# Kernel tuning notes

Hardware: AMD Instinct MI355X
Metric: run time of the kernel (lower is better)

Reference implementation:

```python
import jax, jax.numpy as jnp
import numpy as np

EPS = 1e-5
BLOCKS = 8

def _bn(x, g, b, m, v):
    # eval-mode BatchNorm1d over channel dim of [B, C, T]
    return g[:, None] * (x - m[:, None]) * jax.lax.rsqrt(v[:, None] + EPS) + b[:, None]

def _conv1x1(x, w):
    # x: [B, Cin, T], w: [Cout, Cin] -> [B, Cout, T]
    return jnp.einsum('bct,oc->bot', x, w)

def _dwconv(x, w, dil):
    # x: [B, C, T], w: [C, K] depthwise dilated conv, 'same' padding
    C, K = w.shape
    pad = dil * (K - 1) // 2
    return jax.lax.conv_general_dilated(
        x, w[:, None, :], window_strides=(1,), padding=[(pad, pad)],
        rhs_dilation=(dil,), dimension_numbers=('NCH', 'OIH', 'NCH'),
        feature_group_count=C)

def setup_inputs() -> dict:
    key = jax.random.key(0)
    ks = jax.random.split(key, 16)
    B, Cb, H, T, K = 16, 256, 512, 4096, 3
    d = {}
    d['x'] = jax.random.normal(ks[0], (B, Cb, T), jnp.float32)
    d['bn1_gamma'] = jax.random.uniform(ks[1], (BLOCKS, Cb), jnp.float32)
    d['bn1_beta'] = jax.random.normal(ks[2], (BLOCKS, Cb), jnp.float32)
    d['bn1_mean'] = jax.random.normal(ks[3], (BLOCKS, Cb), jnp.float32)
    d['bn1_var'] = jax.random.uniform(ks[4], (BLOCKS, Cb), jnp.float32)
    d['w1'] = jax.random.normal(ks[5], (BLOCKS, H, Cb), jnp.float32)
    d['bn2_gamma'] = jax.random.uniform(ks[6], (BLOCKS, H), jnp.float32)
    d['bn2_beta'] = jax.random.normal(ks[7], (BLOCKS, H), jnp.float32)
    d['bn2_mean'] = jax.random.normal(ks[8], (BLOCKS, H), jnp.float32)
    d['bn2_var'] = jax.random.uniform(ks[9], (BLOCKS, H), jnp.float32)
    d['dw_w'] = jax.random.normal(ks[10], (BLOCKS, H, K), jnp.float32)
    d['bn3_gamma'] = jax.random.uniform(ks[11], (BLOCKS, H), jnp.float32)
    d['bn3_beta'] = jax.random.normal(ks[12], (BLOCKS, H), jnp.float32)
    d['bn3_mean'] = jax.random.normal(ks[13], (BLOCKS, H), jnp.float32)
    d['bn3_var'] = jax.random.uniform(ks[14], (BLOCKS, H), jnp.float32)
    d['w2'] = jax.random.normal(ks[15], (BLOCKS, Cb, H), jnp.float32)
    return d

def reference(x, bn1_gamma, bn1_beta, bn1_mean, bn1_var, w1,
              bn2_gamma, bn2_beta, bn2_mean, bn2_var, dw_w,
              bn3_gamma, bn3_beta, bn3_mean, bn3_var, w2):
    sign = jnp.sign  # binary activation on inputs and weights
    resid = x
    for i in range(BLOCKS):
        dil = 2 ** i
        h = _bn(resid, bn1_gamma[i], bn1_beta[i], bn1_mean[i], bn1_var[i])
        h = _conv1x1(sign(h), sign(w1[i]))                 # 1x1, Cb -> H
        h = _bn(h, bn2_gamma[i], bn2_beta[i], bn2_mean[i], bn2_var[i])
        h = _dwconv(sign(h), sign(dw_w[i]), dil)           # depthwise dilated
        h = _bn(h, bn3_gamma[i], bn3_beta[i], bn3_mean[i], bn3_var[i])
        h = _conv1x1(sign(h), sign(w2[i]))                 # 1x1, H -> Cb
        resid = resid + h
    return resid
```

## Files before the change

### kernel.cpp

```cpp
#include <hip/hip_runtime.h>
#include <stdint.h>

namespace {
constexpr int Bn  = 16;
constexpr int Cc  = 256;
constexpr int Hn  = 512;
constexpr int Tn  = 4096;
constexpr int CWn = Cc / 32;
constexpr int HWn = Hn / 32;
constexpr int TWn = Tn / 32;
constexpr int TC  = 64;
constexpr float EPSf = 1e-5f;
}

typedef __attribute__((ext_vector_type(4)))  int i32x4;
typedef __attribute__((ext_vector_type(16))) int i32x16;

__global__ __launch_bounds__(256) void setup_kernel(
    const float* __restrict__ bn1g, const float* __restrict__ bn1b,
    const float* __restrict__ bn1m, const float* __restrict__ bn1v,
    const float* __restrict__ w1,
    const float* __restrict__ bn2g, const float* __restrict__ bn2b,
    const float* __restrict__ bn2m, const float* __restrict__ bn2v,
    const float* __restrict__ dww,
    const float* __restrict__ bn3g, const float* __restrict__ bn3b,
    const float* __restrict__ bn3m, const float* __restrict__ bn3v,
    const float* __restrict__ w2,
    float* __restrict__ thr1, float* __restrict__ thr2, float* __restrict__ thr3,
    uint32_t* __restrict__ dws, uint32_t* __restrict__ W1p,
    uint8_t* __restrict__ W1f, int* __restrict__ Sw1, int* __restrict__ T2i,
    uint8_t* __restrict__ W2uf, int* __restrict__ Sw2)
{
  const int idx = blockIdx.x * 256 + threadIdx.x;
  if (idx < 8 * Hn * CWn) {
    const int w = idx & (CWn - 1);
    const int h = idx >> 3;
    const float* src = w1 + (size_t)h * Cc + w * 32;
    uint32_t word = 0;
#pragma unroll
    for (int j = 0; j < 32; ++j) word |= (uint32_t)(src[j] > 0.f) << j;
    W1p[h * CWn + w] = word;
    atomicAdd(&Sw1[h], (int)__popc(word));
    const int blk = h >> 9, hl = h & 511;
    uint32_t* dst = (uint32_t*)(W1f + (size_t)blk * 131072);
#pragma unroll
    for (int q = 0; q < 8; ++q) {
      const uint32_t dw = (((word >> (4 * q)) & 0xFu) * 0x00204081u) & 0x01010101u;
      dst[((w * 2 + (q >> 2)) * 512 + hl) * 4 + (q & 3)] = dw;
    }
  } else {
    const int k = idx - 8 * Hn * CWn;
    const int w = k & (HWn - 1);
    const int c = k >> 4;
    const float* src = w2 + (size_t)c * Hn + w * 32;
    uint32_t word = 0;
#pragma unroll
    for (int j = 0; j < 32; ++j) word |= (uint32_t)(src[j] > 0.f) << j;
    atomicAdd(&Sw2[c], (int)__popc(word));
    const int blk = c >> 8, cl = c & 255;
    uint32_t* dst = (uint32_t*)(W2uf + (size_t)blk * 131072);
#pragma unroll
    for (int q = 0; q < 8; ++q) {
      const uint32_t dw = (((word >> (4 * q)) & 0xFu) * 0x00204081u) & 0x01010101u;
      dst[((w * 2 + (q >> 2)) * 256 + cl) * 4 + (q & 3)] = dw;
    }
  }
  if (idx < 8 * Cc)
    thr1[idx] = bn1m[idx] - bn1b[idx] * sqrtf(bn1v[idx] + EPSf) / bn1g[idx];
  if (idx < 8 * Hn) {
    const float th2 = bn2m[idx] - bn2b[idx] * sqrtf(bn2v[idx] + EPSf) / bn2g[idx];
    thr2[idx] = th2;
    int T;
    if (th2 >= 8.0e6f)       T =  (1 << 24);
    else if (th2 <= -8.0e6f) T = -(1 << 24);
    else if (th2 == th2)     T = (int)floorf(th2) + 1;
    else                     T =  (1 << 24);
    T2i[idx] = T;
    thr3[idx] = bn3m[idx] - bn3b[idx] * sqrtf(bn3v[idx] + EPSf) / bn3g[idx];
    uint32_t dw = 0;
    for (int k2 = 0; k2 < 3; ++k2) dw |= (uint32_t)(dww[(size_t)idx * 3 + k2] > 0.f) << k2;
    dws[idx] = dw;
  }
}

__global__ __launch_bounds__(256) void k1_pack(
    const float* __restrict__ resid, const float* __restrict__ thr1,
    uint32_t* __restrict__ Xp)
{
  const int idx = blockIdx.x * 256 + threadIdx.x;
  const int t  = idx & (Tn - 1);
  const int cw = (idx >> 12) & (CWn - 1);
  const int b  = idx >> 15;
  const float* r = resid + ((size_t)(b * Cc + cw * 32)) * Tn + t;
  uint32_t word = 0;
#pragma unroll
  for (int j = 0; j < 32; ++j)
    word |= (uint32_t)(r[(size_t)j * Tn] > thr1[cw * 32 + j]) << j;
  Xp[((size_t)b * CWn + cw) * Tn + t] = word;
}

__global__ __launch_bounds__(256) void k2_gemm1(
    const uint32_t* __restrict__ Xp, const uint32_t* __restrict__ W1p,
    const float* __restrict__ thr2, uint32_t* __restrict__ Y)
{
  const int bid  = blockIdx.x;
  const int tblk = bid & 15;
  const int og   = (bid >> 4) & 63;
  const int b    = bid >> 10;
  const int t    = tblk * 256 + threadIdx.x;
  const int o    = og * 8;

  const uint32_t* xrow = Xp + (size_t)b * CWn * Tn + t;
  const uint32_t* wrow = W1p + o * CWn;
  int acc[8] = {0, 0, 0, 0, 0, 0, 0, 0};
#pragma unroll
  for (int w = 0; w < CWn; ++w) {
    const uint32_t xw = xrow[(size_t)w * Tn];
#pragma unroll
    for (int r = 0; r < 8; ++r)
      acc[r] += __popc(xw ^ wrow[r * CWn + w]);
  }
  const int lane = threadIdx.x & 63;
#pragma unroll
  for (int r = 0; r < 8; ++r) {
    const float v = (float)(Cc - 2 * acc[r]);
    const uint64_t m = __ballot(v > thr2[o + r]);
    if ((lane & 31) == 0)
      Y[((size_t)b * TWn + (t >> 5)) * Hn + o + r] = (uint32_t)(m >> lane);
  }
}

__global__ __launch_bounds__(512) void k_iter(
    const uint32_t* __restrict__ Yin, const uint32_t* __restrict__ dws,
    const float* __restrict__ thr3,
    const uint8_t* __restrict__ W2uf, const int* __restrict__ Sw2_i,
    const float* __restrict__ rin, float* __restrict__ rout,
    const float* __restrict__ thr1n,
    const uint8_t* __restrict__ W1f_n, const int* __restrict__ Sw1_n,
    const int* __restrict__ T2i_n, uint32_t* __restrict__ Yout,
    int dil, int do_next)
{
  __shared__ __align__(16) uint8_t Zi8[TC * 512];
  __shared__ __align__(16) uint8_t Xi8[TC * 256];
  __shared__ int   Tc[Hn];
  __shared__ float thr1L[Cc];
  __shared__ int   Sw2x2L[Cc];
  __shared__ int   Sx[TC], Sz[TC];

  const int chunk = blockIdx.x & (Tn / TC - 1);
  const int b     = blockIdx.x >> 6;
  const int tid   = threadIdx.x;
  const int lane  = tid & 63;
  const int wid   = __builtin_amdgcn_readfirstlane(tid >> 6);
  const int lh    = lane & 31;
  const int twL   = lane >> 5;
  const int tw0   = chunk * 2;
  const int half  = lane >> 5;

  float rv0[16], rv1[16];
  {
    const int t0 = chunk * TC;
#pragma unroll
    for (int r = 0; r < 16; ++r) {
      const int cr = wid * 32 + (r & 3) + 8 * (r >> 2) + 4 * half;
      const float* rowp = rin + ((size_t)(b * Cc + cr)) * Tn + t0;
      rv0[r] = rowp[lh];
      rv1[r] = rowp[32 + lh];
    }
  }

  if (tid < TC) { Sx[tid] = 0; Sz[tid] = 0; }
  if (tid < Cc) { thr1L[tid] = thr1n[tid]; Sw2x2L[tid] = 2 * Sw2_i[tid]; }
  Tc[tid] = T2i_n[tid] + 2 * Sw1_n[tid] - 256;
  __syncthreads();

  int zcnt = 0;
#pragma unroll
  for (int task = 0; task < 2; ++task) {
    const int hw = wid * 2 + task;
    const int tw = tw0 + twL;
    const int ch = hw * 32 + lh;

    const uint32_t* yb = Yin + (size_t)b * TWn * Hn + ch;
    const uint32_t ycur = yb[(size_t)tw * Hn];
    uint32_t yl, yr, Vl, Vr;
    if (dil >= 32) {
      const int dw = dil >> 5;
      const bool lok = tw >= dw, rok = tw + dw < TWn;
      yl = lok ? yb[(size_t)(tw - dw) * Hn] : 0u;
      yr = rok ? yb[(size_t)(tw + dw) * Hn] : 0u;
      Vl = lok ? ~0u : 0u;
      Vr = rok ? ~0u : 0u;
    } else {
      const uint32_t yp = (tw > 0) ? yb[(size_t)(tw - 1) * Hn] : 0u;
      const uint32_t yn = (tw < TWn - 1) ? yb[(size_t)(tw + 1) * Hn] : 0u;
      yl = (ycur << dil) | ((tw > 0) ? (yp >> (32 - dil)) : 0u);
      yr = (ycur >> dil) | ((tw < TWn - 1) ? (yn << (32 - dil)) : 0u);
      Vl = (tw == 0) ? (~0u << dil) : ~0u;
      Vr = (tw == TWn - 1) ? (~0u >> dil) : ~0u;
    }
    const uint32_t d = dws[ch];
    const uint32_t a  = ((d & 1u) ? yl : ~yl) & Vl;
    const uint32_t bb = (d & 2u) ? ycur : ~ycur;
    const uint32_t c  = ((d & 4u) ? yr : ~yr) & Vr;

    const float thr = thr3[ch];
    const float v3 = (thr + 3.f) * 0.5f;
    const float v2 = (thr + 2.f) * 0.5f;
    const int K3 = (int)(v3 >= 0.f) + (int)(v3 >= 1.f) + (int)(v3 >= 2.f) + (int)(v3 >= 3.f);
    const int K2 = (int)(v2 >= 0.f) + (int)(v2 >= 1.f) + (int)(v2 >= 2.f);

    const uint32_t g1 = a | bb | c;
    const uint32_t g2 = (a & bb) | (c & (a | bb));
    const uint32_t g3 = a & bb & c;
    const uint32_t full = (K3 == 0) ? ~0u : (K3 == 1) ? g1 : (K3 == 2) ? g2
                        : (K3 == 3) ? g3 : 0u;
    const uint32_t lm = (K2 == 0) ? ~0u : (K2 == 1) ? (bb | c) : (K2 == 2) ? (bb & c) : 0u;
    const uint32_t rm = (K2 == 0) ? ~0u : (K2 == 1) ? (a | bb) : (K2 == 2) ? (a & bb) : 0u;

    uint32_t w = (Vl & Vr & full) | (~Vl & lm) | (~Vr & rm);

#pragma unroll
    for (int s = 16; s; s >>= 1) {
      const uint32_t m = 0xFFFFFFFFu / ((1u << s) + 1u);
      const uint32_t o = __shfl_xor(w, s, 64);
      w = ((lane & s) == 0) ? ((w & m) | ((o & m) << s))
                            : ((w & ~m) | ((o & ~m) >> s));
    }
    const int swzA = (lane & 15) << 4;
    uint32_t e[8];
#pragma unroll
    for (int q = 0; q < 8; ++q)
      e[q] = (((w >> (4 * q)) & 0xFu) * 0x00204081u) & 0x01010101u;
    i32x4 v0; v0[0] = e[0]; v0[1] = e[1]; v0[2] = e[2]; v0[3] = e[3];
    i32x4 v1; v1[0] = e[4]; v1[1] = e[5]; v1[2] = e[6]; v1[3] = e[7];
    *(i32x4*)&Zi8[lane * 512 + ((hw * 32)      ^ swzA)] = v0;
    *(i32x4*)&Zi8[lane * 512 + ((hw * 32 + 16) ^ swzA)] = v1;
    zcnt += (int)__popc(w);
  }
  atomicAdd(&Sz[lane], zcnt);
  __syncthreads();

  {
    const int mc   = wid;
    const int lrow = mc * 32 + lh;
    const int t0   = chunk * TC;

    const int swz0 = (lh & 15) << 4;
    i32x16 acc0 = {0,0,0,0, 0,0,0,0, 0,0,0,0, 0,0,0,0};
    i32x16 acc1 = {0,0,0,0, 0,0,0,0, 0,0,0,0, 0,0,0,0};
#pragma unroll
    for (int kg = 0; kg < 2; ++kg) {
      i32x4 afv[8];
#pragma unroll
      for (int kk = 0; kk < 8; ++kk) {
        const int ks = kg * 8 + kk;
        afv[kk] = *(const i32x4*)(W2uf + (((size_t)(ks * 2 + half) * 256 + lrow) * 16));
      }
#pragma unroll
      for (int kk = 0; kk < 8; ++kk) {
        const int ks = kg * 8 + kk;
        const int k0 = ks * 32 + half * 16;
        const i32x4 bf0 = *(const i32x4*)&Zi8[lh * 512 + (k0 ^ swz0)];
        const i32x4 bf1 = *(const i32x4*)&Zi8[(32 + lh) * 512 + (k0 ^ swz0)];
        acc0 = __builtin_amdgcn_mfma_i32_32x32x32_i8(afv[kk], bf0, acc0, 0, 0, 0);
        acc1 = __builtin_amdgcn_mfma_i32_32x32x32_i8(afv[kk], bf1, acc1, 0, 0, 0);
      }
    }

    const int Sz0 = 2 * Sz[lh], Sz1 = 2 * Sz[32 + lh];
    uint32_t dw0[4] = {0,0,0,0}, dw1[4] = {0,0,0,0};
#pragma unroll
    for (int r = 0; r < 16; ++r) {
      const int cr = mc * 32 + (r & 3) + 8 * (r >> 2) + 4 * half;
      const int sw2 = Sw2x2L[cr];
      const float th = thr1L[cr];
      float* orow = rout + ((size_t)(b * Cc + cr)) * Tn + t0;
      const float ro0 = rv0[r] + (float)((acc0[r] << 2) - Sz0 - sw2 + 512);
      const float ro1 = rv1[r] + (float)((acc1[r] << 2) - Sz1 - sw2 + 512);
      orow[lh]      = ro0;
      orow[32 + lh] = ro1;
      dw0[r >> 2] |= (uint32_t)(ro0 > th) << ((r & 3) * 8);
      dw1[r >> 2] |= (uint32_t)(ro1 > th) << ((r & 3) * 8);
    }
    int cnt0 = 0, cnt1 = 0;
#pragma unroll
    for (int g = 0; g < 4; ++g) {
      const int cb = mc * 32 + g * 8 + half * 4;
      *(uint32_t*)&Xi8[lh * 256 + (cb ^ swz0)]        = dw0[g];
      *(uint32_t*)&Xi8[(32 + lh) * 256 + (cb ^ swz0)] = dw1[g];
      cnt0 += __popc(dw0[g]); cnt1 += __popc(dw1[g]);
    }
    atomicAdd(&Sx[lh], cnt0);
    atomicAdd(&Sx[32 + lh], cnt1);
  }
  __syncthreads();

  if (do_next) {
    const int ntile = wid & 1;
    const int mloc  = wid >> 1;
    const int tloc  = ntile * 32 + lh;

    i32x4 bf[8];
#pragma unroll
    for (int ks = 0; ks < 8; ++ks) {
      const int koff = (ks * 32 + half * 16) ^ ((tloc & 15) << 4);
      bf[ks] = *(const i32x4*)&Xi8[tloc * 256 + koff];
    }
    const int Sxv2 = 2 * Sx[tloc];
    uint32_t* yo = Yout + ((size_t)b * TWn + (chunk * 2 + ntile)) * Hn;

#pragma unroll 1
    for (int msup = 0; msup < 4; ++msup) {
      const int row = msup * 128 + mloc * 32 + lh;
      i32x4 afv[8];
#pragma unroll
      for (int ks = 0; ks < 8; ++ks)
        afv[ks] = *(const i32x4*)(W1f_n + (((size_t)(ks * 2 + half) * 512 + row) * 16));
      i32x16 acc = {0,0,0,0, 0,0,0,0, 0,0,0,0, 0,0,0,0};
#pragma unroll
      for (int ks = 0; ks < 8; ++ks)
        acc = __builtin_amdgcn_mfma_i32_32x32x32_i8(afv[ks], bf[ks], acc, 0, 0, 0);

      const int obase = msup * 128 + mloc * 32;
#pragma unroll
      for (int r = 0; r < 16; ++r) {
        const int orow = (r & 3) + 8 * (r >> 2) + 4 * half;
        const int o = obase + orow;
        const uint64_t m = __ballot((acc[r] << 2) >= Tc[o] + Sxv2);
        if ((lane & 31) == 0) yo[o] = (uint32_t)(m >> lane);
      }
    }
  }
}

extern "C" void kernel_launch(void* const* d_in, const int* in_sizes, int n_in,
                              void* d_out, int out_size, void* d_ws, size_t ws_size,
                              hipStream_t stream)
{
  const float* x     = (const float*)d_in[0];
  const float* bn1g  = (const float*)d_in[1];
  const float* bn1b  = (const float*)d_in[2];
  const float* bn1m  = (const float*)d_in[3];
  const float* bn1v  = (const float*)d_in[4];
  const float* w1    = (const float*)d_in[5];
  const float* bn2g  = (const float*)d_in[6];
  const float* bn2b  = (const float*)d_in[7];
  const float* bn2m  = (const float*)d_in[8];
  const float* bn2v  = (const float*)d_in[9];
  const float* dww   = (const float*)d_in[10];
  const float* bn3g  = (const float*)d_in[11];
  const float* bn3b  = (const float*)d_in[12];
  const float* bn3m  = (const float*)d_in[13];
  const float* bn3v  = (const float*)d_in[14];
  const float* w2    = (const float*)d_in[15];
  float* out = (float*)d_out;

  char* ws = (char*)d_ws;
  uint32_t* Xp  = (uint32_t*)(ws);
  uint32_t* Ya  = (uint32_t*)(ws + (2u  << 20));
  uint32_t* Yb  = (uint32_t*)(ws + (6u  << 20));
  uint32_t* W1p = (uint32_t*)(ws + (10u << 20));
  float*    thr1 = (float*)(ws + (10u << 20) + (256u << 10));
  float*    thr2 = thr1 + 8 * Cc;
  float*    thr3 = thr2 + 8 * Hn;
  uint32_t* dws  = (uint32_t*)(thr3 + 8 * Hn);
  uint8_t*  W1f  = (uint8_t*)(ws + (11u << 20));
  int*      Sw1  = (int*)(ws + (12u << 20));
  int*      Sw2  = (int*)(ws + (12u << 20) + (16u << 10));
  int*      T2i  = (int*)(ws + (12u << 20) + (24u << 10));
  uint8_t*  W2uf = (uint8_t*)(ws + (13u << 20));

  hipMemsetAsync(Sw1, 0, (24u << 10), stream);

  setup_kernel<<<256, 256, 0, stream>>>(bn1g, bn1b, bn1m, bn1v, w1,
                                        bn2g, bn2b, bn2m, bn2v, dww,
                                        bn3g, bn3b, bn3m, bn3v, w2,
                                        thr1, thr2, thr3, dws, W1p,
                                        W1f, Sw1, T2i, W2uf, Sw2);

  k1_pack <<<2048,  256, 0, stream>>>(x, thr1, Xp);
  k2_gemm1<<<16384, 256, 0, stream>>>(Xp, W1p, thr2, Ya);

  for (int i = 0; i < 8; ++i) {
    const float* rin = (i == 0) ? x : out;
    const int inext = (i < 7) ? i + 1 : 7;
    const uint32_t* Yin  = (i & 1) ? Yb : Ya;
    uint32_t*       Yout = (i & 1) ? Ya : Yb;
    k_iter<<<1024, 512, 0, stream>>>(Yin, dws + i * Hn, thr3 + i * Hn,
                                     W2uf + (size_t)i * 131072, Sw2 + i * Cc,
                                     rin, out,
                                     thr1 + inext * Cc,
                                     W1f + (size_t)inext * 131072,
                                     Sw1 + inext * Hn, T2i + inext * Hn,
                                     Yout, 1 << i, (i < 7) ? 1 : 0);
  }
}
```

Baseline: 414.5 us.

## Store binarized activations as packed bits in LDS and expand at MFMA load

Result: faster. 394.0 us (-5.0%).

```diff
diff --git a/kernel.cpp b/kernel.cpp
--- a/kernel.cpp
+++ b/kernel.cpp
@@ -15,6 +15,10 @@
 
 typedef __attribute__((ext_vector_type(4)))  int i32x4;
 typedef __attribute__((ext_vector_type(16))) int i32x16;
+
+__device__ __forceinline__ uint32_t nib_expand(uint32_t w, int p) {
+  return (((w >> p) & 0xFu) * 0x00204081u) & 0x01010101u;
+}
 
 __global__ __launch_bounds__(256) void setup_kernel(
     const float* __restrict__ bn1g, const float* __restrict__ bn1b,
@@ -44,10 +48,8 @@
     const int blk = h >> 9, hl = h & 511;
     uint32_t* dst = (uint32_t*)(W1f + (size_t)blk * 131072);
 #pragma unroll
-    for (int q = 0; q < 8; ++q) {
-      const uint32_t dw = (((word >> (4 * q)) & 0xFu) * 0x00204081u) & 0x01010101u;
-      dst[((w * 2 + (q >> 2)) * 512 + hl) * 4 + (q & 3)] = dw;
-    }
+    for (int q = 0; q < 8; ++q)
+      dst[((w * 2 + (q >> 2)) * 512 + hl) * 4 + (q & 3)] = nib_expand(word, 4 * q);
   } else {
     const int k = idx - 8 * Hn * CWn;
     const int w = k & (HWn - 1);
@@ -60,10 +62,8 @@
     const int blk = c >> 8, cl = c & 255;
     uint32_t* dst = (uint32_t*)(W2uf + (size_t)blk * 131072);
 #pragma unroll
-    for (int q = 0; q < 8; ++q) {
-      const uint32_t dw = (((word >> (4 * q)) & 0xFu) * 0x00204081u) & 0x01010101u;
-      dst[((w * 2 + (q >> 2)) * 256 + cl) * 4 + (q & 3)] = dw;
-    }
+    for (int q = 0; q < 8; ++q)
+      dst[((w * 2 + (q >> 2)) * 256 + cl) * 4 + (q & 3)] = nib_expand(word, 4 * q);
   }
   if (idx < 8 * Cc)
     thr1[idx] = bn1m[idx] - bn1b[idx] * sqrtf(bn1v[idx] + EPSf) / bn1g[idx];
@@ -140,8 +140,8 @@
     const int* __restrict__ T2i_n, uint32_t* __restrict__ Yout,
     int dil, int do_next)
 {
-  __shared__ __align__(16) uint8_t Zi8[TC * 512];
-  __shared__ __align__(16) uint8_t Xi8[TC * 256];
+  __shared__ uint32_t ZpL[TC][18];
+  __shared__ uint32_t XpL[TC][9];
   __shared__ int   Tc[Hn];
   __shared__ float thr1L[Cc];
   __shared__ int   Sw2x2L[Cc];
@@ -156,18 +156,6 @@
   const int twL   = lane >> 5;
   const int tw0   = chunk * 2;
   const int half  = lane >> 5;
-
-  float rv0[16], rv1[16];
-  {
-    const int t0 = chunk * TC;
-#pragma unroll
-    for (int r = 0; r < 16; ++r) {
-      const int cr = wid * 32 + (r & 3) + 8 * (r >> 2) + 4 * half;
-      const float* rowp = rin + ((size_t)(b * Cc + cr)) * Tn + t0;
-      rv0[r] = rowp[lh];
-      rv1[r] = rowp[32 + lh];
-    }
-  }
 
   if (tid < TC) { Sx[tid] = 0; Sz[tid] = 0; }
   if (tid < Cc) { thr1L[tid] = thr1n[tid]; Sw2x2L[tid] = 2 * Sw2_i[tid]; }
@@ -227,15 +215,7 @@
       w = ((lane & s) == 0) ? ((w & m) | ((o & m) << s))
                             : ((w & ~m) | ((o & ~m) >> s));
     }
-    const int swzA = (lane & 15) << 4;
-    uint32_t e[8];
-#pragma unroll
-    for (int q = 0; q < 8; ++q)
-      e[q] = (((w >> (4 * q)) & 0xFu) * 0x00204081u) & 0x01010101u;
-    i32x4 v0; v0[0] = e[0]; v0[1] = e[1]; v0[2] = e[2]; v0[3] = e[3];
-    i32x4 v1; v1[0] = e[4]; v1[1] = e[5]; v1[2] = e[6]; v1[3] = e[7];
-    *(i32x4*)&Zi8[lane * 512 + ((hw * 32)      ^ swzA)] = v0;
-    *(i32x4*)&Zi8[lane * 512 + ((hw * 32 + 16) ^ swzA)] = v1;
+    ZpL[lane][hw] = w;
     zcnt += (int)__popc(w);
   }
   atomicAdd(&Sz[lane], zcnt);
@@ -246,7 +226,16 @@
     const int lrow = mc * 32 + lh;
     const int t0   = chunk * TC;
 
-    const int swz0 = (lh & 15) << 4;
+    float rv0[16], rv1[16];
+#pragma unroll
+    for (int r = 0; r < 16; ++r) {
+      const int cr = mc * 32 + (r & 3) + 8 * (r >> 2) + 4 * half;
+      const float* rowp = rin + ((size_t)(b * Cc + cr)) * Tn + t0;
+      rv0[r] = rowp[lh];
+      rv1[r] = rowp[32 + lh];
+    }
+
+    const int hs = half * 16;
     i32x16 acc0 = {0,0,0,0, 0,0,0,0, 0,0,0,0, 0,0,0,0};
     i32x16 acc1 = {0,0,0,0, 0,0,0,0, 0,0,0,0, 0,0,0,0};
 #pragma unroll
@@ -257,22 +246,31 @@
         const int ks = kg * 8 + kk;
         afv[kk] = *(const i32x4*)(W2uf + (((size_t)(ks * 2 + half) * 256 + lrow) * 16));
       }
+      uint32_t z0w[8], z1w[8];
+#pragma unroll
+      for (int j = 0; j < 4; ++j) {
+        *(uint2*)&z0w[2 * j] = *(const uint2*)&ZpL[lh][kg * 8 + 2 * j];
+        *(uint2*)&z1w[2 * j] = *(const uint2*)&ZpL[32 + lh][kg * 8 + 2 * j];
+      }
 #pragma unroll
       for (int kk = 0; kk < 8; ++kk) {
-        const int ks = kg * 8 + kk;
-        const int k0 = ks * 32 + half * 16;
-        const i32x4 bf0 = *(const i32x4*)&Zi8[lh * 512 + (k0 ^ swz0)];
-        const i32x4 bf1 = *(const i32x4*)&Zi8[(32 + lh) * 512 + (k0 ^ swz0)];
+        i32x4 bf0, bf1;
+#pragma unroll
+        for (int q = 0; q < 4; ++q) {
+          bf0[q] = (int)nib_expand(z0w[kk], hs + 4 * q);
+          bf1[q] = (int)nib_expand(z1w[kk], hs + 4 * q);
+        }
         acc0 = __builtin_amdgcn_mfma_i32_32x32x32_i8(afv[kk], bf0, acc0, 0, 0, 0);
         acc1 = __builtin_amdgcn_mfma_i32_32x32x32_i8(afv[kk], bf1, acc1, 0, 0, 0);
       }
     }
 
     const int Sz0 = 2 * Sz[lh], Sz1 = 2 * Sz[32 + lh];
-    uint32_t dw0[4] = {0,0,0,0}, dw1[4] = {0,0,0,0};
+    uint32_t xw0 = 0, xw1 = 0;
 #pragma unroll
     for (int r = 0; r < 16; ++r) {
-      const int cr = mc * 32 + (r & 3) + 8 * (r >> 2) + 4 * half;
+      const int cloc = (r & 3) + 8 * (r >> 2) + 4 * half;
+      const int cr = mc * 32 + cloc;
       const int sw2 = Sw2x2L[cr];
       const float th = thr1L[cr];
       float* orow = rout + ((size_t)(b * Cc + cr)) * Tn + t0;
@@ -280,19 +278,17 @@
       const float ro1 = rv1[r] + (float)((acc1[r] << 2) - Sz1 - sw2 + 512);
       orow[lh]      = ro0;
       orow[32 + lh] = ro1;
-      dw0[r >> 2] |= (uint32_t)(ro0 > th) << ((r & 3) * 8);
-      dw1[r >> 2] |= (uint32_t)(ro1 > th) << ((r & 3) * 8);
-    }
-    int cnt0 = 0, cnt1 = 0;
-#pragma unroll
-    for (int g = 0; g < 4; ++g) {
-      const int cb = mc * 32 + g * 8 + half * 4;
-      *(uint32_t*)&Xi8[lh * 256 + (cb ^ swz0)]        = dw0[g];
-      *(uint32_t*)&Xi8[(32 + lh) * 256 + (cb ^ swz0)] = dw1[g];
-      cnt0 += __popc(dw0[g]); cnt1 += __popc(dw1[g]);
-    }
-    atomicAdd(&Sx[lh], cnt0);
-    atomicAdd(&Sx[32 + lh], cnt1);
+      xw0 |= (uint32_t)(ro0 > th) << cloc;
+      xw1 |= (uint32_t)(ro1 > th) << cloc;
+    }
+    const uint32_t ox0 = xw0 | __shfl_xor(xw0, 32, 64);
+    const uint32_t ox1 = xw1 | __shfl_xor(xw1, 32, 64);
+    if (half == 0) {
+      XpL[lh][mc]      = ox0;
+      XpL[32 + lh][mc] = ox1;
+      atomicAdd(&Sx[lh],      (int)__popc(ox0));
+      atomicAdd(&Sx[32 + lh], (int)__popc(ox1));
+    }
   }
   __syncthreads();
 
@@ -300,12 +296,15 @@
     const int ntile = wid & 1;
     const int mloc  = wid >> 1;
     const int tloc  = ntile * 32 + lh;
+    const int hs    = half * 16;
 
     i32x4 bf[8];
 #pragma unroll
     for (int ks = 0; ks < 8; ++ks) {
-      const int koff = (ks * 32 + half * 16) ^ ((tloc & 15) << 4);
-      bf[ks] = *(const i32x4*)&Xi8[tloc * 256 + koff];
+      const uint32_t xb = XpL[tloc][ks];
+#pragma unroll
+      for (int q = 0; q < 4; ++q)
+        bf[ks][q] = (int)nib_expand(xb, hs + 4 * q);
     }
     const int Sxv2 = 2 * Sx[tloc];
     uint32_t* yo = Yout + ((size_t)b * TWn + (chunk * 2 + ntile)) * Hn;
```
